# Optimization experiments

Measured on AMD Instinct MI355X. Metric: run time of the kernel, lower is better.

## Reference

```python
import jax, jax.numpy as jnp
import numpy as np

BETA = 0.25  # commitment_beta


def setup_inputs() -> dict:
    key = jax.random.key(0)
    k1, k2 = jax.random.split(key)
    B, S, D, K = 4, 2048, 256, 8192
    z_e = jax.random.normal(k1, (B, S, D), dtype=jnp.float32)
    # codebook init ~ uniform(-1/K, 1/K) in the original; scale is irrelevant for correctness,
    # use normal scaled similarly small.
    codebook = jax.random.uniform(k2, (K, D), dtype=jnp.float32, minval=-1.0 / K, maxval=1.0 / K)
    return {"z_e": z_e, "codebook": codebook}


def reference(z_e, codebook):
    B, S, D = z_e.shape
    flat = z_e.reshape(-1, D)  # [N, D], N = B*S
    distances = (
        jnp.sum(flat * flat, axis=1, keepdims=True)
        - 2.0 * (flat @ codebook.T)
        + jnp.sum(codebook * codebook, axis=1)[None, :]
    )
    indices = jnp.argmin(distances, axis=1)  # [N]
    z_q = codebook[indices].reshape(B, S, D)
    codebook_loss = jnp.mean((jax.lax.stop_gradient(z_e) - z_q) ** 2)
    commitment_loss = jnp.mean((z_e - jax.lax.stop_gradient(z_q)) ** 2)
    vq_loss = codebook_loss + BETA * commitment_loss
    # straight-through estimator
    z_q_st = z_e + jax.lax.stop_gradient(z_q - z_e)
    return z_q_st, indices.reshape(B, S), vq_loss
```

## Files before the change

### kernel.cpp

```cpp
#include <hip/hip_runtime.h>
#include <stdint.h>

#define N_ROWS  8192
#define DIM     256
#define K_CODES 8192
#define SPLITK  8
#define KS      1024
#define NT      128
#define LSLOTS  16
#define GSLOTS  8
#define MARGIN_ACC 1.0e-4f

typedef unsigned long long u64;
typedef unsigned short u16;
typedef short s16x8 __attribute__((ext_vector_type(8)));
typedef float f32x4 __attribute__((ext_vector_type(4)));

__device__ __forceinline__ u64 u64min(u64 a, u64 b) { return a < b ? a : b; }

__device__ __forceinline__ u16 f2bf(float f) {
    unsigned u = __float_as_uint(f);
    u += 0x7fffu + ((u >> 16) & 1u);
    return (u16)(u >> 16);
}

__device__ __forceinline__ void gld16(void* lds, const void* g) {
    __builtin_amdgcn_global_load_lds(
        (const __attribute__((address_space(1))) unsigned int*)g,
        (__attribute__((address_space(3))) unsigned int*)lds, 16, 0, 0);
}

__device__ __forceinline__ void block_barrier() {
    asm volatile("" ::: "memory");
    __builtin_amdgcn_s_barrier();
    asm volatile("" ::: "memory");
}

__global__ __launch_bounds__(256) void vq_prep(const float* __restrict__ z_e,
                                               const float* __restrict__ cb,
                                               u16* __restrict__ zb,
                                               u16* __restrict__ cbb,
                                               float* __restrict__ xnorm,
                                               float* __restrict__ cnorm) {
    int wid  = (blockIdx.x * 256 + threadIdx.x) >> 6;
    int lane = threadIdx.x & 63;
    const float* src; u16* d16; float* dn;
    if (wid < N_ROWS) { src = z_e + (size_t)wid * DIM; d16 = zb + (size_t)wid * DIM; dn = xnorm + wid; }
    else              { int k = wid - N_ROWS;
                        src = cb  + (size_t)k   * DIM; d16 = cbb + (size_t)k * DIM; dn = cnorm + k; }
    float4 v = *(const float4*)(src + lane * 4);
    ushort4 h;
    h.x = f2bf(v.x); h.y = f2bf(v.y); h.z = f2bf(v.z); h.w = f2bf(v.w);
    *(ushort4*)(d16 + lane * 4) = h;
    float s = (v.x * v.x + v.y * v.y) + (v.z * v.z + v.w * v.w);
#pragma unroll
    for (int off = 1; off < 64; off <<= 1)
        s += __shfl_xor(s, off, 64);
    if (lane == 0) *dn = s;
}

__global__ __launch_bounds__(256, 2) void vq_mfma(const u16* __restrict__ zb,
                                                  const u16* __restrict__ cbb,
                                                  int* __restrict__ cand_cnt,
                                                  int* __restrict__ cand_idx,
                                                  float* __restrict__ cand_dot) {
    __shared__ u16   Cs[2][128 * 64];
    __shared__ float lcd[128 * LSLOTS];
    __shared__ int   lci[128 * LSLOTS];
    __shared__ int   lcnt[128];
    __shared__ float gmaxs[128];

    const int tid   = threadIdx.x;
    const int lane  = tid & 63;
    const int wave  = tid >> 6;
    const int quad  = lane >> 4;
    const int l16   = lane & 15;
    const int split = blockIdx.x;
    const int n0    = blockIdx.y * 128;

    if (tid < 128) lcnt[tid] = 0;

    const int srow8  = lane >> 3;
    const int schunk = lane & 7;
    const int ssw    = (schunk ^ srow8) * 8;
    const u16* csrc  = cbb + (size_t)split * KS * DIM + (size_t)srow8 * DIM + ssw;

    s16x8 af[2][8];
#pragma unroll
    for (int i = 0; i < 2; i++) {
        const u16* p = zb + (size_t)(n0 + wave * 32 + i * 16 + l16) * DIM + quad * 8;
#pragma unroll
        for (int s = 0; s < 8; s++)
            af[i][s] = *(const s16x8*)(p + s * 32);
    }

    auto STAGE = [&](int s, int slot) {
        const u16* src = csrc + (size_t)(s >> 2) * (NT * DIM) + (s & 3) * 64;
#pragma unroll
        for (int t = 0; t < 4; t++) {
            int rg = wave * 4 + t;
            gld16(&Cs[slot][rg * 512], src + (size_t)rg * (8 * DIM));
        }
    };

    float runmax[8];
#pragma unroll
    for (int t = 0; t < 8; t++) runmax[t] = -3.0e38f;

    STAGE(0, 0);
    asm volatile("s_waitcnt vmcnt(0) lgkmcnt(0)" ::: "memory");
    block_barrier();

    for (int kt = 0; kt < 8; kt++) {
        const int kbase = split * KS + kt * NT;
        f32x4 acc[2][8];
#pragma unroll
        for (int i = 0; i < 2; i++)
#pragma unroll
            for (int j = 0; j < 8; j++)
#pragma unroll
                for (int e = 0; e < 4; e++) acc[i][j][e] = 0.0f;

#pragma unroll
        for (int kc = 0; kc < 4; kc++) {
            const int it = (kt << 2) | kc;
            if (it < 31) STAGE(it + 1, (it + 1) & 1);

            const u16* cbuf = &Cs[it & 1][0];
#pragma unroll
            for (int ks = 0; ks < 2; ks++) {
                s16x8 bfr[8];
#pragma unroll
                for (int j = 0; j < 8; j++)
                    bfr[j] = *(const s16x8*)&cbuf[(j * 16 + l16) * 64 +
                                                  (((ks << 2) | quad) ^ (l16 & 7)) * 8];
#pragma unroll
                for (int i = 0; i < 2; i++)
#pragma unroll
                    for (int j = 0; j < 8; j++)
                        acc[i][j] = __builtin_amdgcn_mfma_f32_16x16x32_bf16(
                            af[i][kc * 2 + ks], bfr[j], acc[i][j], 0, 0, 0);
            }

            if (it < 31) {
                asm volatile("s_waitcnt vmcnt(0) lgkmcnt(0)" ::: "memory");
                block_barrier();
            }
        }

#pragma unroll
        for (int i = 0; i < 2; i++)
#pragma unroll
            for (int r = 0; r < 4; r++) {
                float m = fmaxf(fmaxf(fmaxf(acc[i][0][r], acc[i][1][r]),
                                      fmaxf(acc[i][2][r], acc[i][3][r])),
                                fmaxf(fmaxf(acc[i][4][r], acc[i][5][r]),
                                      fmaxf(acc[i][6][r], acc[i][7][r])));
                m = fmaxf(m, __shfl_xor(m, 1, 64));
                m = fmaxf(m, __shfl_xor(m, 2, 64));
                m = fmaxf(m, __shfl_xor(m, 4, 64));
                m = fmaxf(m, __shfl_xor(m, 8, 64));
                runmax[i * 4 + r] = fmaxf(runmax[i * 4 + r], m);
                float thr = runmax[i * 4 + r] - MARGIN_ACC;
                int rl = wave * 32 + i * 16 + quad * 4 + r;
#pragma unroll
                for (int j = 0; j < 8; j++) {
                    float d = acc[i][j][r];
                    if (d >= thr) {
                        int pos = atomicAdd(&lcnt[rl], 1);
                        if (pos < LSLOTS) {
                            lcd[rl * LSLOTS + pos] = d;
                            lci[rl * LSLOTS + pos] = kbase + j * 16 + l16;
                        }
                    }
                }
            }
    }

    if (l16 == 0) {
#pragma unroll
        for (int i = 0; i < 2; i++)
#pragma unroll
            for (int r = 0; r < 4; r++)
                gmaxs[wave * 32 + i * 16 + quad * 4 + r] = runmax[i * 4 + r];
    }
    __syncthreads();

    if (tid < 128) {
        int n   = n0 + tid;
        int cnt = lcnt[tid]; if (cnt > LSLOTS) cnt = LSLOTS;
        float thrf = gmaxs[tid] - MARGIN_ACC;
        float bd[GSLOTS]; int bi[GSLOTS];
        int w = 0;
        for (int s = 0; s < cnt; s++) {
            float d = lcd[tid * LSLOTS + s];
            if (d < thrf) continue;
            if (w < GSLOTS) { bd[w] = d; bi[w] = lci[tid * LSLOTS + s]; w++; }
            else {
                int mn = 0;
#pragma unroll
                for (int k = 1; k < GSLOTS; k++) if (bd[k] < bd[mn]) mn = k;
                if (d > bd[mn]) { bd[mn] = d; bi[mn] = lci[tid * LSLOTS + s]; }
            }
        }
        int base = (split * N_ROWS + n) * GSLOTS;
        for (int k = 0; k < w; k++) {
            cand_idx[base + k] = bi[k];
            cand_dot[base + k] = bd[k];
        }
        cand_cnt[split * N_ROWS + n] = w;
    }
}

__global__ __launch_bounds__(256) void vq_finalize(const float* __restrict__ z_e,
                                                   const float* __restrict__ cb,
                                                   const float* __restrict__ xnorm,
                                                   const float* __restrict__ cnorm,
                                                   const int* __restrict__ cand_cnt,
                                                   const int* __restrict__ cand_idx,
                                                   const float* __restrict__ cand_dot,
                                                   float* __restrict__ out_zq,
                                                   float* __restrict__ out_idx,
                                                   float* __restrict__ rowloss) {
    const int n    = blockIdx.x * 4 + (threadIdx.x >> 6);
    const int lane = threadIdx.x & 63;

    int   myidx = -1;
    float mydot = -3.0e38f;
    int t = 0;
#pragma unroll
    for (int s = 0; s < SPLITK; s++) {
        int c = cand_cnt[s * N_ROWS + n];
        if (lane >= t && lane < t + c) {
            myidx = cand_idx[(s * N_ROWS + n) * GSLOTS + (lane - t)];
            mydot = cand_dot[(s * N_ROWS + n) * GSLOTS + (lane - t)];
        }
        t += c;
    }

    float mg = mydot;
#pragma unroll
    for (int off = 1; off < 64; off <<= 1)
        mg = fmaxf(mg, __shfl_xor(mg, off, 64));

    u64 key = ~0ULL;
    if (myidx >= 0 && mydot >= mg - MARGIN_ACC) {
        const float* xr = z_e + (size_t)n * DIM;
        const float* cr = cb + (size_t)myidx * DIM;
        float acc = 0.0f;
#pragma unroll 8
        for (int d = 0; d < DIM; d++)
            acc = __builtin_fmaf(xr[d], cr[d], acc);
        float dist = __builtin_fmaf(-2.0f, acc, xnorm[n]) + cnorm[myidx];
        key = ((u64)__float_as_uint(dist) << 32) | (unsigned)myidx;
    }
#pragma unroll
    for (int off = 1; off < 64; off <<= 1)
        key = u64min(key, __shfl_xor(key, off, 64));

    int idx = (int)(unsigned)(key & 0xffffffffu);
    if (key == ~0ULL) idx = 0;

    float4 x = *(const float4*)(z_e + (size_t)n * DIM + lane * 4);
    float4 c = *(const float4*)(cb + (size_t)idx * DIM + lane * 4);
    float4 st;
    st.x = x.x + (c.x - x.x); st.y = x.y + (c.y - x.y);
    st.z = x.z + (c.z - x.z); st.w = x.w + (c.w - x.w);
    *(float4*)(out_zq + (size_t)n * DIM + lane * 4) = st;

    float d0 = x.x - c.x, d1 = x.y - c.y, d2 = x.z - c.z, d3 = x.w - c.w;
    float s2 = (d0 * d0 + d1 * d1) + (d2 * d2 + d3 * d3);
#pragma unroll
    for (int off = 1; off < 64; off <<= 1)
        s2 += __shfl_xor(s2, off, 64);
    if (lane == 0) {
        rowloss[n] = s2;
        out_idx[n] = (float)idx;
    }
}

__global__ __launch_bounds__(256) void vq_loss(const float* __restrict__ rowloss,
                                               float* __restrict__ out_loss) {
    __shared__ double sd[256];
    double s = 0.0;
    for (int i = threadIdx.x; i < N_ROWS; i += 256) s += (double)rowloss[i];
    sd[threadIdx.x] = s;
    __syncthreads();
    for (int off = 128; off; off >>= 1) {
        if (threadIdx.x < off) sd[threadIdx.x] += sd[threadIdx.x + off];
        __syncthreads();
    }
    if (threadIdx.x == 0) {
        double mean = sd[0] / (double)((size_t)N_ROWS * DIM);
        out_loss[0] = (float)(1.25 * mean);
    }
}

extern "C" void kernel_launch(void* const* d_in, const int* in_sizes, int n_in,
                              void* d_out, int out_size, void* d_ws, size_t ws_size,
                              hipStream_t stream) {
    const float* z_e = (const float*)d_in[0];
    const float* cb  = (const float*)d_in[1];

    float* out   = (float*)d_out;
    float* zq    = out;
    float* oidx  = out + (size_t)N_ROWS * DIM;
    float* oloss = oidx + N_ROWS;

    u16*   zb       = (u16*)d_ws;
    u16*   cbb      = zb + (size_t)N_ROWS * DIM;
    float* xnorm    = (float*)(cbb + (size_t)K_CODES * DIM);
    float* cnorm    = xnorm + N_ROWS;
    float* rowloss  = cnorm + K_CODES;
    int*   cand_cnt = (int*)(rowloss + N_ROWS);
    int*   cand_idx = cand_cnt + N_ROWS * SPLITK;
    float* cand_dot = (float*)(cand_idx + (size_t)N_ROWS * SPLITK * GSLOTS);

    vq_prep    <<<(N_ROWS + K_CODES) / 4, 256, 0, stream>>>(z_e, cb, zb, cbb, xnorm, cnorm);
    vq_mfma    <<<dim3(SPLITK, N_ROWS / 128), 256, 0, stream>>>(zb, cbb, cand_cnt, cand_idx, cand_dot);
    vq_finalize<<<N_ROWS / 4, 256, 0, stream>>>(z_e, cb, xnorm, cnorm, cand_cnt, cand_idx, cand_dot, zq, oidx, rowloss);
    vq_loss    <<<1, 256, 0, stream>>>(rowloss, oloss);
}
```

Baseline: 172.2 us.

## Double split-K factor, pack candidates into 32-bit words, fuse loss reduction

Raises the codebook split from 8 to 16 slices of 512 codes, so the MFMA kernel launches twice as many blocks and each does half the work. Candidate dot products and indices are packed into one 32-bit word (bf16 dot plus 13-bit index), which halves candidate traffic; the finalize margin is widened to cover the lower precision. The separate single-block loss kernel is removed. Its work moves into finalize through double atomics and a last-block counter, which saves a launch but adds atomic contention and means twice as many candidates per row to scan.

```diff
diff --git a/kernel.cpp b/kernel.cpp
--- a/kernel.cpp
+++ b/kernel.cpp
@@ -4,12 +4,13 @@
 #define N_ROWS  8192
 #define DIM     256
 #define K_CODES 8192
-#define SPLITK  8
-#define KS      1024
+#define SPLITK  16
+#define KS      512
 #define NT      128
-#define LSLOTS  16
+#define LSLOTS  15
 #define GSLOTS  8
 #define MARGIN_ACC 1.0e-4f
+#define MARGIN_FIN 2.5e-4f
 
 typedef unsigned long long u64;
 typedef unsigned short u16;
@@ -41,7 +42,10 @@
                                                u16* __restrict__ zb,
                                                u16* __restrict__ cbb,
                                                float* __restrict__ xnorm,
-                                               float* __restrict__ cnorm) {
+                                               float* __restrict__ cnorm,
+                                               double* __restrict__ loss_acc,
+                                               unsigned* __restrict__ loss_cnt) {
+    if (blockIdx.x == 0 && threadIdx.x == 0) { *loss_acc = 0.0; *loss_cnt = 0u; }
     int wid  = (blockIdx.x * 256 + threadIdx.x) >> 6;
     int lane = threadIdx.x & 63;
     const float* src; u16* d16; float* dn;
@@ -62,8 +66,7 @@
 __global__ __launch_bounds__(256, 2) void vq_mfma(const u16* __restrict__ zb,
                                                   const u16* __restrict__ cbb,
                                                   int* __restrict__ cand_cnt,
-                                                  int* __restrict__ cand_idx,
-                                                  float* __restrict__ cand_dot) {
+                                                  unsigned* __restrict__ cand_pk) {
     __shared__ u16   Cs[2][128 * 64];
     __shared__ float lcd[128 * LSLOTS];
     __shared__ int   lci[128 * LSLOTS];
@@ -111,7 +114,7 @@
     asm volatile("s_waitcnt vmcnt(0) lgkmcnt(0)" ::: "memory");
     block_barrier();
 
-    for (int kt = 0; kt < 8; kt++) {
+    for (int kt = 0; kt < KS / NT; kt++) {
         const int kbase = split * KS + kt * NT;
         f32x4 acc[2][8];
 #pragma unroll
@@ -124,7 +127,7 @@
 #pragma unroll
         for (int kc = 0; kc < 4; kc++) {
             const int it = (kt << 2) | kc;
-            if (it < 31) STAGE(it + 1, (it + 1) & 1);
+            if (it < 15) STAGE(it + 1, (it + 1) & 1);
 
             const u16* cbuf = &Cs[it & 1][0];
 #pragma unroll
@@ -142,7 +145,7 @@
                             af[i][kc * 2 + ks], bfr[j], acc[i][j], 0, 0, 0);
             }
 
-            if (it < 31) {
+            if (it < 15) {
                 asm volatile("s_waitcnt vmcnt(0) lgkmcnt(0)" ::: "memory");
                 block_barrier();
             }
@@ -204,10 +207,8 @@
             }
         }
         int base = (split * N_ROWS + n) * GSLOTS;
-        for (int k = 0; k < w; k++) {
-            cand_idx[base + k] = bi[k];
-            cand_dot[base + k] = bd[k];
-        }
+        for (int k = 0; k < w; k++)
+            cand_pk[base + k] = ((unsigned)f2bf(bd[k]) << 16) | (unsigned)bi[k];
         cand_cnt[split * N_ROWS + n] = w;
     }
 }
@@ -217,12 +218,15 @@
                                                    const float* __restrict__ xnorm,
                                                    const float* __restrict__ cnorm,
                                                    const int* __restrict__ cand_cnt,
-                                                   const int* __restrict__ cand_idx,
-                                                   const float* __restrict__ cand_dot,
+                                                   const unsigned* __restrict__ cand_pk,
                                                    float* __restrict__ out_zq,
                                                    float* __restrict__ out_idx,
-                                                   float* __restrict__ rowloss) {
-    const int n    = blockIdx.x * 4 + (threadIdx.x >> 6);
+                                                   float* __restrict__ out_loss,
+                                                   double* __restrict__ loss_acc,
+                                                   unsigned* __restrict__ loss_cnt) {
+    __shared__ float ssum[4];
+    const int wv   = threadIdx.x >> 6;
+    const int n    = blockIdx.x * 4 + wv;
     const int lane = threadIdx.x & 63;
 
     int   myidx = -1;
@@ -232,8 +236,9 @@
     for (int s = 0; s < SPLITK; s++) {
         int c = cand_cnt[s * N_ROWS + n];
         if (lane >= t && lane < t + c) {
-            myidx = cand_idx[(s * N_ROWS + n) * GSLOTS + (lane - t)];
-            mydot = cand_dot[(s * N_ROWS + n) * GSLOTS + (lane - t)];
+            unsigned key = cand_pk[(s * N_ROWS + n) * GSLOTS + (lane - t)];
+            myidx = (int)(key & 0x1FFFu);
+            mydot = __uint_as_float(key & 0xFFFF0000u);
         }
         t += c;
     }
@@ -244,7 +249,7 @@
         mg = fmaxf(mg, __shfl_xor(mg, off, 64));
 
     u64 key = ~0ULL;
-    if (myidx >= 0 && mydot >= mg - MARGIN_ACC) {
+    if (myidx >= 0 && mydot >= mg - MARGIN_FIN) {
         const float* xr = z_e + (size_t)n * DIM;
         const float* cr = cb + (size_t)myidx * DIM;
         float acc = 0.0f;
@@ -274,25 +279,21 @@
     for (int off = 1; off < 64; off <<= 1)
         s2 += __shfl_xor(s2, off, 64);
     if (lane == 0) {
-        rowloss[n] = s2;
         out_idx[n] = (float)idx;
-    }
-}
-
-__global__ __launch_bounds__(256) void vq_loss(const float* __restrict__ rowloss,
-                                               float* __restrict__ out_loss) {
-    __shared__ double sd[256];
-    double s = 0.0;
-    for (int i = threadIdx.x; i < N_ROWS; i += 256) s += (double)rowloss[i];
-    sd[threadIdx.x] = s;
+        ssum[wv] = s2;
+    }
     __syncthreads();
-    for (int off = 128; off; off >>= 1) {
-        if (threadIdx.x < off) sd[threadIdx.x] += sd[threadIdx.x + off];
-        __syncthreads();
-    }
+
     if (threadIdx.x == 0) {
-        double mean = sd[0] / (double)((size_t)N_ROWS * DIM);
-        out_loss[0] = (float)(1.25 * mean);
+        double bs = ((double)ssum[0] + (double)ssum[1]) +
+                    ((double)ssum[2] + (double)ssum[3]);
+        atomicAdd(loss_acc, bs);
+        __threadfence();
+        unsigned old = atomicAdd(loss_cnt, 1u);
+        if (old == (N_ROWS / 4 - 1)) {
+            double tot = atomicAdd(loss_acc, 0.0);
+            out_loss[0] = (float)(1.25 * tot / (double)((size_t)N_ROWS * DIM));
+        }
     }
 }
 
@@ -307,17 +308,18 @@
     float* oidx  = out + (size_t)N_ROWS * DIM;
     float* oloss = oidx + N_ROWS;
 
-    u16*   zb       = (u16*)d_ws;
-    u16*   cbb      = zb + (size_t)N_ROWS * DIM;
-    float* xnorm    = (float*)(cbb + (size_t)K_CODES * DIM);
-    float* cnorm    = xnorm + N_ROWS;
-    float* rowloss  = cnorm + K_CODES;
-    int*   cand_cnt = (int*)(rowloss + N_ROWS);
-    int*   cand_idx = cand_cnt + N_ROWS * SPLITK;
-    float* cand_dot = (float*)(cand_idx + (size_t)N_ROWS * SPLITK * GSLOTS);
-
-    vq_prep    <<<(N_ROWS + K_CODES) / 4, 256, 0, stream>>>(z_e, cb, zb, cbb, xnorm, cnorm);
-    vq_mfma    <<<dim3(SPLITK, N_ROWS / 128), 256, 0, stream>>>(zb, cbb, cand_cnt, cand_idx, cand_dot);
-    vq_finalize<<<N_ROWS / 4, 256, 0, stream>>>(z_e, cb, xnorm, cnorm, cand_cnt, cand_idx, cand_dot, zq, oidx, rowloss);
-    vq_loss    <<<1, 256, 0, stream>>>(rowloss, oloss);
-}
+    u16*      zb       = (u16*)d_ws;
+    u16*      cbb      = zb + (size_t)N_ROWS * DIM;
+    float*    xnorm    = (float*)(cbb + (size_t)K_CODES * DIM);
+    float*    cnorm    = xnorm + N_ROWS;
+    int*      cand_cnt = (int*)(cnorm + K_CODES);
+    unsigned* cand_pk  = (unsigned*)(cand_cnt + N_ROWS * SPLITK);
+    double*   loss_acc = (double*)(cand_pk + (size_t)N_ROWS * SPLITK * GSLOTS);
+    unsigned* loss_cnt = (unsigned*)(loss_acc + 1);
+
+    vq_prep    <<<(N_ROWS + K_CODES) / 4, 256, 0, stream>>>(z_e, cb, zb, cbb, xnorm, cnorm,
+                                                            loss_acc, loss_cnt);
+    vq_mfma    <<<dim3(SPLITK, N_ROWS / 128), 256, 0, stream>>>(zb, cbb, cand_cnt, cand_pk);
+    vq_finalize<<<N_ROWS / 4, 256, 0, stream>>>(z_e, cb, xnorm, cnorm, cand_cnt, cand_pk,
+                                                zq, oidx, oloss, loss_acc, loss_cnt);
+}
```

Result: slower. 229.5 us (+33.3%).
